# Performance work log

Hardware: AMD Instinct MI355X
Metric: run time of the kernel (lower is better)

The kernel has to match this reference:

```python
import jax, jax.numpy as jnp
import numpy as np

NUM_HEADS = 32
NUM_KV_HEADS = 8
HEAD_SIZE = 128
SCALE = 0.08838834764831845  # 1/sqrt(128)
BATCH = 32
MAX_BLOCKS_PER_SEQ = 128
BLOCK_SIZE = 16
NUM_BLOCKS = BATCH * MAX_BLOCKS_PER_SEQ  # 4096
MAX_CTX = MAX_BLOCKS_PER_SEQ * BLOCK_SIZE  # 2048


def setup_inputs() -> dict:
    key = jax.random.key(0)
    ks = jax.random.split(key, 8)
    query = jax.random.normal(ks[0], (BATCH, 1, NUM_HEADS * HEAD_SIZE), dtype=jnp.float32)
    k_new = jax.random.normal(ks[1], (BATCH, 1, NUM_KV_HEADS * HEAD_SIZE), dtype=jnp.float32)
    v_new = jax.random.normal(ks[2], (BATCH, 1, NUM_KV_HEADS * HEAD_SIZE), dtype=jnp.float32)
    key_cache = jax.random.normal(ks[3], (NUM_BLOCKS, NUM_KV_HEADS, HEAD_SIZE, BLOCK_SIZE), dtype=jnp.float32)
    value_cache = jax.random.normal(ks[4], (NUM_BLOCKS, NUM_KV_HEADS, HEAD_SIZE, BLOCK_SIZE), dtype=jnp.float32)
    # each sequence owns a contiguous stripe of blocks, accessed through the table
    block_tables = jnp.arange(NUM_BLOCKS, dtype=jnp.int32).reshape(BATCH, MAX_BLOCKS_PER_SEQ)
    context_lens = jax.random.randint(ks[5], (BATCH,), 1, MAX_CTX + 1, dtype=jnp.int32)
    # slot for the newly-decoded token (position context_len-1)
    last = context_lens - 1
    blk_idx = block_tables[jnp.arange(BATCH), last // BLOCK_SIZE]
    slot_mapping = (blk_idx * BLOCK_SIZE + last % BLOCK_SIZE).reshape(BATCH, 1).astype(jnp.int32)
    return {
        "query": query, "key": k_new, "value": v_new,
        "key_cache": key_cache, "value_cache": value_cache,
        "block_tables": block_tables, "context_lens": context_lens,
        "slot_mapping": slot_mapping,
    }


def reference(query, key, value, key_cache, value_cache, block_tables, context_lens, slot_mapping):
    B = query.shape[0]
    block_size = value_cache.shape[3]
    q_per_kv = NUM_HEADS // NUM_KV_HEADS

    # --- reshape_and_cache: write new k/v into paged caches at slot_mapping ---
    slots = slot_mapping.reshape(-1)                       # [B] (seq_len=1 decode)
    blk = slots // block_size
    off = slots % block_size
    k_new = key.reshape(B, NUM_KV_HEADS, HEAD_SIZE)
    v_new = value.reshape(B, NUM_KV_HEADS, HEAD_SIZE)
    key_cache = key_cache.at[blk, :, :, off].set(k_new)
    value_cache = value_cache.at[blk, :, :, off].set(v_new)

    # --- paged_attention_v1: gather blocks via block_tables, masked softmax ---
    # [B, MB, KVH, D, bs] -> [B, MB, bs, KVH, D] -> [B, T, KVH, D]
    K = jnp.moveaxis(key_cache[block_tables], -1, 2).reshape(B, -1, NUM_KV_HEADS, HEAD_SIZE)
    V = jnp.moveaxis(value_cache[block_tables], -1, 2).reshape(B, -1, NUM_KV_HEADS, HEAD_SIZE)
    T = K.shape[1]

    q = query.reshape(B, NUM_KV_HEADS, q_per_kv, HEAD_SIZE)
    scores = jnp.einsum('bkqd,btkd->bkqt', q, K) * SCALE   # [B, KVH, Qper, T]
    valid = (jnp.arange(T, dtype=jnp.int32)[None, :] < context_lens[:, None])
    scores = jnp.where(valid[:, None, None, :], scores, jnp.finfo(scores.dtype).min)
    probs = jax.nn.softmax(scores, axis=-1)
    out = jnp.einsum('bkqt,btkd->bkqd', probs, V)          # [B, KVH, Qper, D]
    return out.reshape(B, 1, NUM_HEADS * HEAD_SIZE)
```

## Files before the change

kernel.cpp:

```cpp
#include <hip/hip_runtime.h>
#include <float.h>

#define NUM_HEADS    32
#define NUM_KV_HEADS 8
#define HEAD_SIZE    128
#define Q_PER_KV     4
#define BLOCK_SZ     16
#define MAX_BLOCKS   128
#define SCALE        0.08838834764831845f

#define CHUNK_BLOCKS 8
#define CHUNK_TOK    (CHUNK_BLOCKS * BLOCK_SZ)
#define NCHUNK       (MAX_BLOCKS / CHUNK_BLOCKS)
#define WS_STRIDE    528

typedef float v4f __attribute__((ext_vector_type(4)));

__global__ __launch_bounds__(64, 4)
void paged_attn_chunk(const float* __restrict__ query,
                      const float* __restrict__ key_cache,
                      const float* __restrict__ value_cache,
                      const int* __restrict__ block_tables,
                      const int* __restrict__ context_lens,
                      float* __restrict__ ws) {
    const int c   = blockIdx.x;
    const int h   = blockIdx.y;
    const int b   = blockIdx.z;
    const int tid = threadIdx.x;

    const int ctx = context_lens[b];
    const int nb  = (ctx + BLOCK_SZ - 1) / BLOCK_SZ;
    const int b0  = c * CHUNK_BLOCKS;
    if (b0 >= nb) return;
    const int nbl  = min(nb - b0, CHUNK_BLOCKS);
    const int last = ctx - 1;

    __shared__ float q_lds[Q_PER_KV * HEAD_SIZE];
    __shared__ float s_lds[Q_PER_KV * CHUNK_TOK];

    {
        const v4f* qg = reinterpret_cast<const v4f*>(
            query + ((size_t)b * NUM_HEADS + h * Q_PER_KV) * HEAD_SIZE);
        v4f* ql = reinterpret_cast<v4f*>(q_lds);
        ql[tid]      = qg[tid]      * SCALE;
        ql[tid + 64] = qg[tid + 64] * SCALE;
    }
    __syncthreads();

    {
        const int o   = tid & 3;
        const int bi8 = (tid >> 2) & 7;
        const int rep = tid >> 5;
        v4f acc[Q_PER_KV];
        #pragma unroll
        for (int qh = 0; qh < Q_PER_KV; ++qh) acc[qh] = (v4f)0.f;

        if (bi8 < nbl) {
            const int phys = block_tables[b * MAX_BLOCKS + b0 + bi8];
            const v4f* kp = reinterpret_cast<const v4f*>(key_cache) +
                            ((size_t)phys * NUM_KV_HEADS + h) * (HEAD_SIZE * BLOCK_SZ / 4);
            const v4f* q4 = reinterpret_cast<const v4f*>(q_lds);
            #pragma unroll 4
            for (int d4 = rep * 16; d4 < rep * 16 + 16; ++d4) {
                v4f k[4];
                #pragma unroll
                for (int dd = 0; dd < 4; ++dd) k[dd] = kp[d4 * 16 + dd * 4 + o];
                #pragma unroll
                for (int qh = 0; qh < Q_PER_KV; ++qh) {
                    const v4f qv = q4[qh * (HEAD_SIZE / 4) + d4];
                    #pragma unroll
                    for (int dd = 0; dd < 4; ++dd) acc[qh] += qv[dd] * k[dd];
                }
            }
        }
        #pragma unroll
        for (int qh = 0; qh < Q_PER_KV; ++qh) {
            #pragma unroll
            for (int j = 0; j < 4; ++j)
                acc[qh][j] += __shfl_xor(acc[qh][j], 32);
        }
        if (rep == 0) {
            const int t0 = bi8 * BLOCK_SZ + o * 4;
            const int g0 = b0 * BLOCK_SZ + t0;
            #pragma unroll
            for (int qh = 0; qh < Q_PER_KV; ++qh) {
                v4f sv;
                #pragma unroll
                for (int j = 0; j < 4; ++j) {
                    const int g = g0 + j;
                    sv[j] = (bi8 < nbl && g < ctx && g != last) ? acc[qh][j] : -FLT_MAX;
                }
                *reinterpret_cast<v4f*>(&s_lds[qh * CHUNK_TOK + t0]) = sv;
            }
        }
    }
    __syncthreads();

    float* wsp = ws + (((size_t)b * NUM_KV_HEADS + h) * NCHUNK + c) * WS_STRIDE;
    #pragma unroll
    for (int qh = 0; qh < Q_PER_KV; ++qh) {
        const float s0 = s_lds[qh * CHUNK_TOK + tid];
        const float s1 = s_lds[qh * CHUNK_TOK + tid + 64];
        float m = fmaxf(s0, s1);
        #pragma unroll
        for (int off = 32; off; off >>= 1) m = fmaxf(m, __shfl_xor(m, off));
        const float p0 = (s0 == -FLT_MAX) ? 0.f : __expf(s0 - m);
        const float p1 = (s1 == -FLT_MAX) ? 0.f : __expf(s1 - m);
        s_lds[qh * CHUNK_TOK + tid]      = p0;
        s_lds[qh * CHUNK_TOK + tid + 64] = p1;
        float l = p0 + p1;
        #pragma unroll
        for (int off = 32; off; off >>= 1) l += __shfl_xor(l, off);
        if (tid == 0) { wsp[qh] = m; wsp[Q_PER_KV + qh] = l; }
    }
    __syncthreads();

    {
        const int d0 = tid, d1 = tid + 64;
        float acc0[Q_PER_KV] = {0.f, 0.f, 0.f, 0.f};
        float acc1[Q_PER_KV] = {0.f, 0.f, 0.f, 0.f};
        for (int bil = 0; bil < nbl; ++bil) {
            const int phys = block_tables[b * MAX_BLOCKS + b0 + bil];
            const v4f* vp = reinterpret_cast<const v4f*>(value_cache) +
                            ((size_t)phys * NUM_KV_HEADS + h) * (HEAD_SIZE * BLOCK_SZ / 4);
            v4f vv0[4], vv1[4];
            #pragma unroll
            for (int j = 0; j < 4; ++j) { vv0[j] = vp[d0 * 4 + j]; vv1[j] = vp[d1 * 4 + j]; }
            #pragma unroll
            for (int qh = 0; qh < Q_PER_KV; ++qh) {
                const v4f* pq = reinterpret_cast<const v4f*>(
                    &s_lds[qh * CHUNK_TOK + bil * BLOCK_SZ]);
                #pragma unroll
                for (int j = 0; j < 4; ++j) {
                    const v4f p = pq[j];
                    acc0[qh] += p[0]*vv0[j][0] + p[1]*vv0[j][1] + p[2]*vv0[j][2] + p[3]*vv0[j][3];
                    acc1[qh] += p[0]*vv1[j][0] + p[1]*vv1[j][1] + p[2]*vv1[j][2] + p[3]*vv1[j][3];
                }
            }
        }
        float* wo = wsp + 2 * Q_PER_KV;
        #pragma unroll
        for (int qh = 0; qh < Q_PER_KV; ++qh) {
            wo[qh * HEAD_SIZE + d0] = acc0[qh];
            wo[qh * HEAD_SIZE + d1] = acc1[qh];
        }
    }
}

__global__ __launch_bounds__(512, 2)
void paged_attn_reduce(const float* __restrict__ query,
                       const float* __restrict__ k_new,
                       const float* __restrict__ v_new,
                       const int* __restrict__ context_lens,
                       const float* __restrict__ ws,
                       float* __restrict__ out) {
    const int h   = blockIdx.x;
    const int b   = blockIdx.y;
    const int tid = threadIdx.x;

    __shared__ float snew_lds[Q_PER_KV];

    const int ctx = context_lens[b];
    const int nb  = (ctx + BLOCK_SZ - 1) / BLOCK_SZ;
    const int nch = (nb + CHUNK_BLOCKS - 1) / CHUNK_BLOCKS;

    if (tid < 4 * 64) {
        const int w = tid >> 6, lane = tid & 63;
        const float* qp = query + ((size_t)b * NUM_HEADS + h * Q_PER_KV + w) * HEAD_SIZE;
        const float* kn = k_new + ((size_t)b * NUM_KV_HEADS + h) * HEAD_SIZE;
        float v = qp[lane] * kn[lane] + qp[lane + 64] * kn[lane + 64];
        #pragma unroll
        for (int off = 32; off; off >>= 1) v += __shfl_xor(v, off);
        if (lane == 0) snew_lds[w] = v * SCALE;
    }
    __syncthreads();

    const int qh = tid >> 7, d = tid & 127;
    const float* wsb = ws + ((size_t)b * NUM_KV_HEADS + h) * NCHUNK * WS_STRIDE;

    float M = -FLT_MAX, L = 0.f, acc = 0.f;
    for (int c = 0; c < nch; ++c) {
        const float* wsp = wsb + (size_t)c * WS_STRIDE;
        const float mc = wsp[qh];
        const float lc = wsp[Q_PER_KV + qh];
        const float oc = wsp[2 * Q_PER_KV + qh * HEAD_SIZE + d];
        const float nM = fmaxf(M, mc);
        const float eM = __expf(M - nM), ec = __expf(mc - nM);
        acc = acc * eM + oc * ec;
        L   = L   * eM + lc * ec;
        M   = nM;
    }
    {
        const float s  = snew_lds[qh];
        const float nM = fmaxf(M, s);
        const float eM = __expf(M - nM), es = __expf(s - nM);
        const float vn = v_new[((size_t)b * NUM_KV_HEADS + h) * HEAD_SIZE + d];
        acc = acc * eM + es * vn;
        L   = L   * eM + es;
    }
    out[((size_t)b * NUM_HEADS + h * Q_PER_KV + qh) * HEAD_SIZE + d] = acc / L;
}

extern "C" void kernel_launch(void* const* d_in, const int* in_sizes, int n_in,
                              void* d_out, int out_size, void* d_ws, size_t ws_size,
                              hipStream_t stream) {
    const float* query       = (const float*)d_in[0];
    const float* k_new       = (const float*)d_in[1];
    const float* v_new       = (const float*)d_in[2];
    const float* key_cache   = (const float*)d_in[3];
    const float* value_cache = (const float*)d_in[4];
    const int*   block_tables  = (const int*)d_in[5];
    const int*   context_lens  = (const int*)d_in[6];
    float* out = (float*)d_out;
    float* ws  = (float*)d_ws;

    const int batch = in_sizes[6];

    dim3 g1(NCHUNK, NUM_KV_HEADS, batch);
    paged_attn_chunk<<<g1, 64, 0, stream>>>(query, key_cache, value_cache,
                                            block_tables, context_lens, ws);
    dim3 g2(NUM_KV_HEADS, batch);
    paged_attn_reduce<<<g2, 512, 0, stream>>>(query, k_new, v_new,
                                              context_lens, ws, out);
}
```

Measured before the change: 73.01 us.

## Fuse chunk and reduce kernels with atomic last-block reduction, larger chunks

Merges the split-KV chunk kernel and the reduction kernel into one launch. The last finishing chunk for each (batch, kv-head), detected through an atomic counter in the workspace, performs the log-sum-exp merge and folds in the new token. It also doubles chunk size to 16 blocks, drops the two-way split of the QK dot product, prefetches the next V block, and reorders the grid so chunks are the slowest dimension. This saves a launch and the inter-kernel gap, at the cost of a memset launch, fences and atomics, and fewer, longer workgroups.

```diff
diff --git a/kernel.cpp b/kernel.cpp
--- a/kernel.cpp
+++ b/kernel.cpp
@@ -9,23 +9,28 @@
 #define MAX_BLOCKS   128
 #define SCALE        0.08838834764831845f
 
-#define CHUNK_BLOCKS 8
+#define CHUNK_BLOCKS 16
 #define CHUNK_TOK    (CHUNK_BLOCKS * BLOCK_SZ)
 #define NCHUNK       (MAX_BLOCKS / CHUNK_BLOCKS)
 #define WS_STRIDE    528
+#define CTR_FLT_OFF  (8u * 1024u * 1024u)
 
 typedef float v4f __attribute__((ext_vector_type(4)));
 
 __global__ __launch_bounds__(64, 4)
-void paged_attn_chunk(const float* __restrict__ query,
+void paged_attn_fused(const float* __restrict__ query,
+                      const float* __restrict__ k_new,
+                      const float* __restrict__ v_new,
                       const float* __restrict__ key_cache,
                       const float* __restrict__ value_cache,
                       const int* __restrict__ block_tables,
                       const int* __restrict__ context_lens,
-                      float* __restrict__ ws) {
-    const int c   = blockIdx.x;
-    const int h   = blockIdx.y;
-    const int b   = blockIdx.z;
+                      float* __restrict__ ws,
+                      int* __restrict__ ctr,
+                      float* __restrict__ out) {
+    const int h   = blockIdx.x;
+    const int b   = blockIdx.y;
+    const int c   = blockIdx.z;
     const int tid = threadIdx.x;
 
     const int ctx = context_lens[b];
@@ -33,10 +38,12 @@
     const int b0  = c * CHUNK_BLOCKS;
     if (b0 >= nb) return;
     const int nbl  = min(nb - b0, CHUNK_BLOCKS);
+    const int nch  = (nb + CHUNK_BLOCKS - 1) / CHUNK_BLOCKS;
     const int last = ctx - 1;
 
     __shared__ float q_lds[Q_PER_KV * HEAD_SIZE];
     __shared__ float s_lds[Q_PER_KV * CHUNK_TOK];
+    __shared__ int   old_lds;
 
     {
         const v4f* qg = reinterpret_cast<const v4f*>(
@@ -48,20 +55,18 @@
     __syncthreads();
 
     {
+        const int bil = tid >> 2;
         const int o   = tid & 3;
-        const int bi8 = (tid >> 2) & 7;
-        const int rep = tid >> 5;
-        v4f acc[Q_PER_KV];
-        #pragma unroll
-        for (int qh = 0; qh < Q_PER_KV; ++qh) acc[qh] = (v4f)0.f;
-
-        if (bi8 < nbl) {
-            const int phys = block_tables[b * MAX_BLOCKS + b0 + bi8];
+        if (bil < nbl) {
+            const int phys = block_tables[b * MAX_BLOCKS + b0 + bil];
             const v4f* kp = reinterpret_cast<const v4f*>(key_cache) +
                             ((size_t)phys * NUM_KV_HEADS + h) * (HEAD_SIZE * BLOCK_SZ / 4);
             const v4f* q4 = reinterpret_cast<const v4f*>(q_lds);
+            v4f acc[Q_PER_KV];
+            #pragma unroll
+            for (int qh = 0; qh < Q_PER_KV; ++qh) acc[qh] = (v4f)0.f;
             #pragma unroll 4
-            for (int d4 = rep * 16; d4 < rep * 16 + 16; ++d4) {
+            for (int d4 = 0; d4 < HEAD_SIZE / 4; ++d4) {
                 v4f k[4];
                 #pragma unroll
                 for (int dd = 0; dd < 4; ++dd) k[dd] = kp[d4 * 16 + dd * 4 + o];
@@ -72,15 +77,7 @@
                     for (int dd = 0; dd < 4; ++dd) acc[qh] += qv[dd] * k[dd];
                 }
             }
-        }
-        #pragma unroll
-        for (int qh = 0; qh < Q_PER_KV; ++qh) {
-            #pragma unroll
-            for (int j = 0; j < 4; ++j)
-                acc[qh][j] += __shfl_xor(acc[qh][j], 32);
-        }
-        if (rep == 0) {
-            const int t0 = bi8 * BLOCK_SZ + o * 4;
+            const int t0 = bil * BLOCK_SZ + o * 4;
             const int g0 = b0 * BLOCK_SZ + t0;
             #pragma unroll
             for (int qh = 0; qh < Q_PER_KV; ++qh) {
@@ -88,7 +85,7 @@
                 #pragma unroll
                 for (int j = 0; j < 4; ++j) {
                     const int g = g0 + j;
-                    sv[j] = (bi8 < nbl && g < ctx && g != last) ? acc[qh][j] : -FLT_MAX;
+                    sv[j] = (g < ctx && g != last) ? acc[qh][j] : -FLT_MAX;
                 }
                 *reinterpret_cast<v4f*>(&s_lds[qh * CHUNK_TOK + t0]) = sv;
             }
@@ -96,36 +93,51 @@
     }
     __syncthreads();
 
+    const int d0 = tid, d1 = tid + 64;
+    v4f cur0[4], cur1[4];
+    {
+        const int phys = block_tables[b * MAX_BLOCKS + b0];
+        const v4f* vp = reinterpret_cast<const v4f*>(value_cache) +
+                        ((size_t)phys * NUM_KV_HEADS + h) * (HEAD_SIZE * BLOCK_SZ / 4);
+        #pragma unroll
+        for (int j = 0; j < 4; ++j) { cur0[j] = vp[d0 * 4 + j]; cur1[j] = vp[d1 * 4 + j]; }
+    }
+
     float* wsp = ws + (((size_t)b * NUM_KV_HEADS + h) * NCHUNK + c) * WS_STRIDE;
-    #pragma unroll
-    for (int qh = 0; qh < Q_PER_KV; ++qh) {
-        const float s0 = s_lds[qh * CHUNK_TOK + tid];
-        const float s1 = s_lds[qh * CHUNK_TOK + tid + 64];
-        float m = fmaxf(s0, s1);
-        #pragma unroll
-        for (int off = 32; off; off >>= 1) m = fmaxf(m, __shfl_xor(m, off));
-        const float p0 = (s0 == -FLT_MAX) ? 0.f : __expf(s0 - m);
-        const float p1 = (s1 == -FLT_MAX) ? 0.f : __expf(s1 - m);
-        s_lds[qh * CHUNK_TOK + tid]      = p0;
-        s_lds[qh * CHUNK_TOK + tid + 64] = p1;
-        float l = p0 + p1;
-        #pragma unroll
-        for (int off = 32; off; off >>= 1) l += __shfl_xor(l, off);
-        if (tid == 0) { wsp[qh] = m; wsp[Q_PER_KV + qh] = l; }
-    }
-    __syncthreads();
-
-    {
-        const int d0 = tid, d1 = tid + 64;
+    {
+        const int T = nbl * BLOCK_SZ;
+        #pragma unroll
+        for (int qh = 0; qh < Q_PER_KV; ++qh) {
+            float m = -FLT_MAX;
+            for (int t = tid; t < T; t += 64) m = fmaxf(m, s_lds[qh * CHUNK_TOK + t]);
+            #pragma unroll
+            for (int off = 32; off; off >>= 1) m = fmaxf(m, __shfl_xor(m, off));
+            float l = 0.f;
+            for (int t = tid; t < T; t += 64) {
+                const float s = s_lds[qh * CHUNK_TOK + t];
+                const float p = (s == -FLT_MAX) ? 0.f : __expf(s - m);
+                s_lds[qh * CHUNK_TOK + t] = p;
+                l += p;
+            }
+            #pragma unroll
+            for (int off = 32; off; off >>= 1) l += __shfl_xor(l, off);
+            if (tid == 0) { wsp[qh] = m; wsp[Q_PER_KV + qh] = l; }
+        }
+    }
+    __syncthreads();
+
+    {
         float acc0[Q_PER_KV] = {0.f, 0.f, 0.f, 0.f};
         float acc1[Q_PER_KV] = {0.f, 0.f, 0.f, 0.f};
         for (int bil = 0; bil < nbl; ++bil) {
-            const int phys = block_tables[b * MAX_BLOCKS + b0 + bil];
-            const v4f* vp = reinterpret_cast<const v4f*>(value_cache) +
-                            ((size_t)phys * NUM_KV_HEADS + h) * (HEAD_SIZE * BLOCK_SZ / 4);
-            v4f vv0[4], vv1[4];
-            #pragma unroll
-            for (int j = 0; j < 4; ++j) { vv0[j] = vp[d0 * 4 + j]; vv1[j] = vp[d1 * 4 + j]; }
+            v4f nxt0[4], nxt1[4];
+            if (bil + 1 < nbl) {
+                const int physn = block_tables[b * MAX_BLOCKS + b0 + bil + 1];
+                const v4f* vpn = reinterpret_cast<const v4f*>(value_cache) +
+                                 ((size_t)physn * NUM_KV_HEADS + h) * (HEAD_SIZE * BLOCK_SZ / 4);
+                #pragma unroll
+                for (int j = 0; j < 4; ++j) { nxt0[j] = vpn[d0 * 4 + j]; nxt1[j] = vpn[d1 * 4 + j]; }
+            }
             #pragma unroll
             for (int qh = 0; qh < Q_PER_KV; ++qh) {
                 const v4f* pq = reinterpret_cast<const v4f*>(
@@ -133,9 +145,13 @@
                 #pragma unroll
                 for (int j = 0; j < 4; ++j) {
                     const v4f p = pq[j];
-                    acc0[qh] += p[0]*vv0[j][0] + p[1]*vv0[j][1] + p[2]*vv0[j][2] + p[3]*vv0[j][3];
-                    acc1[qh] += p[0]*vv1[j][0] + p[1]*vv1[j][1] + p[2]*vv1[j][2] + p[3]*vv1[j][3];
+                    acc0[qh] += p[0]*cur0[j][0] + p[1]*cur0[j][1] + p[2]*cur0[j][2] + p[3]*cur0[j][3];
+                    acc1[qh] += p[0]*cur1[j][0] + p[1]*cur1[j][1] + p[2]*cur1[j][2] + p[3]*cur1[j][3];
                 }
+            }
+            if (bil + 1 < nbl) {
+                #pragma unroll
+                for (int j = 0; j < 4; ++j) { cur0[j] = nxt0[j]; cur1[j] = nxt1[j]; }
             }
         }
         float* wo = wsp + 2 * Q_PER_KV;
@@ -145,60 +161,59 @@
             wo[qh * HEAD_SIZE + d1] = acc1[qh];
         }
     }
-}
-
-__global__ __launch_bounds__(512, 2)
-void paged_attn_reduce(const float* __restrict__ query,
-                       const float* __restrict__ k_new,
-                       const float* __restrict__ v_new,
-                       const int* __restrict__ context_lens,
-                       const float* __restrict__ ws,
-                       float* __restrict__ out) {
-    const int h   = blockIdx.x;
-    const int b   = blockIdx.y;
-    const int tid = threadIdx.x;
-
-    __shared__ float snew_lds[Q_PER_KV];
-
-    const int ctx = context_lens[b];
-    const int nb  = (ctx + BLOCK_SZ - 1) / BLOCK_SZ;
-    const int nch = (nb + CHUNK_BLOCKS - 1) / CHUNK_BLOCKS;
-
-    if (tid < 4 * 64) {
-        const int w = tid >> 6, lane = tid & 63;
-        const float* qp = query + ((size_t)b * NUM_HEADS + h * Q_PER_KV + w) * HEAD_SIZE;
+
+    __syncthreads();
+    __threadfence();
+    if (tid == 0) old_lds = atomicAdd(&ctr[b * NUM_KV_HEADS + h], 1);
+    __syncthreads();
+    if (old_lds != nch - 1) return;
+    __threadfence();
+
+    {
+        const float* wsb = ws + ((size_t)b * NUM_KV_HEADS + h) * NCHUNK * WS_STRIDE;
+        float M[Q_PER_KV], L[Q_PER_KV], a0[Q_PER_KV], a1[Q_PER_KV];
+        #pragma unroll
+        for (int qh = 0; qh < Q_PER_KV; ++qh) { M[qh] = -FLT_MAX; L[qh] = 0.f; a0[qh] = 0.f; a1[qh] = 0.f; }
+
+        for (int cc = 0; cc < nch; ++cc) {
+            const float* rp = wsb + (size_t)cc * WS_STRIDE;
+            #pragma unroll
+            for (int qh = 0; qh < Q_PER_KV; ++qh) {
+                const float mc = rp[qh];
+                const float lc = rp[Q_PER_KV + qh];
+                const float o0 = rp[2 * Q_PER_KV + qh * HEAD_SIZE + d0];
+                const float o1 = rp[2 * Q_PER_KV + qh * HEAD_SIZE + d1];
+                const float nM = fmaxf(M[qh], mc);
+                const float eM = __expf(M[qh] - nM), ec = __expf(mc - nM);
+                a0[qh] = a0[qh] * eM + o0 * ec;
+                a1[qh] = a1[qh] * eM + o1 * ec;
+                L[qh]  = L[qh]  * eM + lc * ec;
+                M[qh]  = nM;
+            }
+        }
         const float* kn = k_new + ((size_t)b * NUM_KV_HEADS + h) * HEAD_SIZE;
-        float v = qp[lane] * kn[lane] + qp[lane + 64] * kn[lane + 64];
-        #pragma unroll
-        for (int off = 32; off; off >>= 1) v += __shfl_xor(v, off);
-        if (lane == 0) snew_lds[w] = v * SCALE;
-    }
-    __syncthreads();
-
-    const int qh = tid >> 7, d = tid & 127;
-    const float* wsb = ws + ((size_t)b * NUM_KV_HEADS + h) * NCHUNK * WS_STRIDE;
-
-    float M = -FLT_MAX, L = 0.f, acc = 0.f;
-    for (int c = 0; c < nch; ++c) {
-        const float* wsp = wsb + (size_t)c * WS_STRIDE;
-        const float mc = wsp[qh];
-        const float lc = wsp[Q_PER_KV + qh];
-        const float oc = wsp[2 * Q_PER_KV + qh * HEAD_SIZE + d];
-        const float nM = fmaxf(M, mc);
-        const float eM = __expf(M - nM), ec = __expf(mc - nM);
-        acc = acc * eM + oc * ec;
-        L   = L   * eM + lc * ec;
-        M   = nM;
-    }
-    {
-        const float s  = snew_lds[qh];
-        const float nM = fmaxf(M, s);
-        const float eM = __expf(M - nM), es = __expf(s - nM);
-        const float vn = v_new[((size_t)b * NUM_KV_HEADS + h) * HEAD_SIZE + d];
-        acc = acc * eM + es * vn;
-        L   = L   * eM + es;
-    }
-    out[((size_t)b * NUM_HEADS + h * Q_PER_KV + qh) * HEAD_SIZE + d] = acc / L;
+        const float* vn = v_new + ((size_t)b * NUM_KV_HEADS + h) * HEAD_SIZE;
+        const float kn0 = kn[d0], kn1 = kn[d1];
+        const float vn0 = vn[d0], vn1 = vn[d1];
+        #pragma unroll
+        for (int qh = 0; qh < Q_PER_KV; ++qh) {
+            float s = q_lds[qh * HEAD_SIZE + d0] * kn0 + q_lds[qh * HEAD_SIZE + d1] * kn1;
+            #pragma unroll
+            for (int off = 32; off; off >>= 1) s += __shfl_xor(s, off);
+            const float nM = fmaxf(M[qh], s);
+            const float eM = __expf(M[qh] - nM), es = __expf(s - nM);
+            a0[qh] = a0[qh] * eM + es * vn0;
+            a1[qh] = a1[qh] * eM + es * vn1;
+            L[qh]  = L[qh]  * eM + es;
+        }
+        float* ob = out + ((size_t)b * NUM_HEADS + h * Q_PER_KV) * HEAD_SIZE;
+        #pragma unroll
+        for (int qh = 0; qh < Q_PER_KV; ++qh) {
+            const float inv = 1.0f / L[qh];
+            ob[qh * HEAD_SIZE + d0] = a0[qh] * inv;
+            ob[qh * HEAD_SIZE + d1] = a1[qh] * inv;
+        }
+    }
 }
 
 extern "C" void kernel_launch(void* const* d_in, const int* in_sizes, int n_in,
@@ -213,13 +228,15 @@
     const int*   context_lens  = (const int*)d_in[6];
     float* out = (float*)d_out;
     float* ws  = (float*)d_ws;
+    int*   ctr = (int*)(ws + CTR_FLT_OFF);
 
     const int batch = in_sizes[6];
 
-    dim3 g1(NCHUNK, NUM_KV_HEADS, batch);
-    paged_attn_chunk<<<g1, 64, 0, stream>>>(query, key_cache, value_cache,
-                                            block_tables, context_lens, ws);
-    dim3 g2(NUM_KV_HEADS, batch);
-    paged_attn_reduce<<<g2, 512, 0, stream>>>(query, k_new, v_new,
-                                              context_lens, ws, out);
+    hipMemsetAsync(ctr, 0, batch * NUM_KV_HEADS * sizeof(int), stream);
+
+    dim3 g(NUM_KV_HEADS, batch, NCHUNK);
+    paged_attn_fused<<<g, 64, 0, stream>>>(query, k_new, v_new,
+                                           key_cache, value_cache,
+                                           block_tables, context_lens,
+                                           ws, ctr, out);
 }
```

Measured after the change: 237.5 us. 225% more time.

## Double chunk size and assign one KV block per thread group in QK

Applied to the files above, without the earlier changes.

Raises the chunk from 8 to 16 blocks, which halves the number of chunk workgroups and the partial results the reduce kernel has to merge. The QK stage now gives each group of four threads a whole block over the full head dimension, which removes the cross-half shuffle reduction. The softmax loops now cover only the valid tokens. In exchange there are fewer workgroups to spread across the GPU, and each thread runs a longer serial dot-product loop with less memory-level parallelism.

```diff
diff --git a/kernel.cpp b/kernel.cpp
--- a/kernel.cpp
+++ b/kernel.cpp
@@ -9,7 +9,7 @@
 #define MAX_BLOCKS   128
 #define SCALE        0.08838834764831845f
 
-#define CHUNK_BLOCKS 8
+#define CHUNK_BLOCKS 16
 #define CHUNK_TOK    (CHUNK_BLOCKS * BLOCK_SZ)
 #define NCHUNK       (MAX_BLOCKS / CHUNK_BLOCKS)
 #define WS_STRIDE    528
@@ -48,20 +48,18 @@
     __syncthreads();
 
     {
+        const int bil = tid >> 2;
         const int o   = tid & 3;
-        const int bi8 = (tid >> 2) & 7;
-        const int rep = tid >> 5;
-        v4f acc[Q_PER_KV];
-        #pragma unroll
-        for (int qh = 0; qh < Q_PER_KV; ++qh) acc[qh] = (v4f)0.f;
-
-        if (bi8 < nbl) {
-            const int phys = block_tables[b * MAX_BLOCKS + b0 + bi8];
+        if (bil < nbl) {
+            const int phys = block_tables[b * MAX_BLOCKS + b0 + bil];
             const v4f* kp = reinterpret_cast<const v4f*>(key_cache) +
                             ((size_t)phys * NUM_KV_HEADS + h) * (HEAD_SIZE * BLOCK_SZ / 4);
             const v4f* q4 = reinterpret_cast<const v4f*>(q_lds);
+            v4f acc[Q_PER_KV];
+            #pragma unroll
+            for (int qh = 0; qh < Q_PER_KV; ++qh) acc[qh] = (v4f)0.f;
             #pragma unroll 4
-            for (int d4 = rep * 16; d4 < rep * 16 + 16; ++d4) {
+            for (int d4 = 0; d4 < HEAD_SIZE / 4; ++d4) {
                 v4f k[4];
                 #pragma unroll
                 for (int dd = 0; dd < 4; ++dd) k[dd] = kp[d4 * 16 + dd * 4 + o];
@@ -72,46 +70,42 @@
                     for (int dd = 0; dd < 4; ++dd) acc[qh] += qv[dd] * k[dd];
                 }
             }
-        }
+            const int t0 = bil * BLOCK_SZ + o * 4;
+            const int g0 = b0 * BLOCK_SZ + t0;
+            #pragma unroll
+            for (int qh = 0; qh < Q_PER_KV; ++qh) {
+                v4f sv;
+                #pragma unroll
+                for (int j = 0; j < 4; ++j) {
+                    const int g = g0 + j;
+                    sv[j] = (g < ctx && g != last) ? acc[qh][j] : -FLT_MAX;
+                }
+                *reinterpret_cast<v4f*>(&s_lds[qh * CHUNK_TOK + t0]) = sv;
+            }
+        }
+    }
+    __syncthreads();
+
+    float* wsp = ws + (((size_t)b * NUM_KV_HEADS + h) * NCHUNK + c) * WS_STRIDE;
+    {
+        const int T = nbl * BLOCK_SZ;
         #pragma unroll
         for (int qh = 0; qh < Q_PER_KV; ++qh) {
-            #pragma unroll
-            for (int j = 0; j < 4; ++j)
-                acc[qh][j] += __shfl_xor(acc[qh][j], 32);
-        }
-        if (rep == 0) {
-            const int t0 = bi8 * BLOCK_SZ + o * 4;
-            const int g0 = b0 * BLOCK_SZ + t0;
-            #pragma unroll
-            for (int qh = 0; qh < Q_PER_KV; ++qh) {
-                v4f sv;
-                #pragma unroll
-                for (int j = 0; j < 4; ++j) {
-                    const int g = g0 + j;
-                    sv[j] = (bi8 < nbl && g < ctx && g != last) ? acc[qh][j] : -FLT_MAX;
-                }
-                *reinterpret_cast<v4f*>(&s_lds[qh * CHUNK_TOK + t0]) = sv;
-            }
-        }
-    }
-    __syncthreads();
-
-    float* wsp = ws + (((size_t)b * NUM_KV_HEADS + h) * NCHUNK + c) * WS_STRIDE;
-    #pragma unroll
-    for (int qh = 0; qh < Q_PER_KV; ++qh) {
-        const float s0 = s_lds[qh * CHUNK_TOK + tid];
-        const float s1 = s_lds[qh * CHUNK_TOK + tid + 64];
-        float m = fmaxf(s0, s1);
-        #pragma unroll
-        for (int off = 32; off; off >>= 1) m = fmaxf(m, __shfl_xor(m, off));
-        const float p0 = (s0 == -FLT_MAX) ? 0.f : __expf(s0 - m);
-        const float p1 = (s1 == -FLT_MAX) ? 0.f : __expf(s1 - m);
-        s_lds[qh * CHUNK_TOK + tid]      = p0;
-        s_lds[qh * CHUNK_TOK + tid + 64] = p1;
-        float l = p0 + p1;
-        #pragma unroll
-        for (int off = 32; off; off >>= 1) l += __shfl_xor(l, off);
-        if (tid == 0) { wsp[qh] = m; wsp[Q_PER_KV + qh] = l; }
+            float m = -FLT_MAX;
+            for (int t = tid; t < T; t += 64) m = fmaxf(m, s_lds[qh * CHUNK_TOK + t]);
+            #pragma unroll
+            for (int off = 32; off; off >>= 1) m = fmaxf(m, __shfl_xor(m, off));
+            float l = 0.f;
+            for (int t = tid; t < T; t += 64) {
+                const float s = s_lds[qh * CHUNK_TOK + t];
+                const float p = (s == -FLT_MAX) ? 0.f : __expf(s - m);
+                s_lds[qh * CHUNK_TOK + t] = p;
+                l += p;
+            }
+            #pragma unroll
+            for (int off = 32; off; off >>= 1) l += __shfl_xor(l, off);
+            if (tid == 0) { wsp[qh] = m; wsp[Q_PER_KV + qh] = l; }
+        }
     }
     __syncthreads();
 
```

Result: slower. 79.52 us (+8.9%).
